# Performance work log

Hardware: AMD Instinct MI355X
Metric: run time of the kernel (lower is better)

## Reference

```python
import jax, jax.numpy as jnp
import numpy as np

COMMITMENT_COST = 0.25


def setup_inputs() -> dict:
    key = jax.random.key(0)
    kx, ke = jax.random.split(key)
    B, T, D = 64, 512, 256
    Q, K = 8, 1024
    x = jax.random.normal(kx, (B, T, D), dtype=jnp.float32)
    # matches nn.Embedding init uniform_(-1/codebook_size, 1/codebook_size)
    embeddings = jax.random.uniform(ke, (Q, K, D), dtype=jnp.float32,
                                    minval=-1.0 / K, maxval=1.0 / K)
    return {"x": x, "embeddings": embeddings}


def _vq_layer(residual, emb):
    # residual: [B,T,D], emb: [K,D]
    B, T, D = residual.shape
    flat = residual.reshape(-1, D)                               # [N,D]
    # squared distances via ||a||^2 + ||b||^2 - 2 a.b
    dist = (jnp.sum(flat * flat, axis=1, keepdims=True)
            + jnp.sum(emb * emb, axis=1)
            - 2.0 * (flat @ emb.T))                              # [N,K]
    idx = jnp.argmin(dist, axis=1)                               # [N]
    q = emb[idx].reshape(residual.shape)                         # gather == one_hot @ emb
    sg = jax.lax.stop_gradient
    e_latent = jnp.mean((sg(q) - residual) ** 2)
    q_latent = jnp.mean((q - sg(residual)) ** 2)
    loss = q_latent + COMMITMENT_COST * e_latent
    quantized = residual + sg(q - residual)                      # straight-through
    return quantized, loss, idx.reshape(B, T)


def reference(x, embeddings):
    # Residual VQ: sequentially quantize the residual with each codebook.
    def step(residual, emb):
        quantized, loss, idx = _vq_layer(residual, emb)
        return residual - quantized, (loss, idx)

    residual, (losses, indices) = jax.lax.scan(step, x, embeddings)
    output = x - residual                                        # [B,T,D]
    total_loss = jnp.sum(losses)
    return output, total_loss, indices                           # indices: [Q,B,T]
```

## Files before the change

### kernel.cpp

```cpp
#include <hip/hip_runtime.h>

#define NTOK   32768
#define DDIM   256
#define KCODES 1024
#define QLAYERS 8

#define MT     64
#define NCHUNK 32
#define NCH    (KCODES / NCHUNK)
#define DELTA  4e-4f
#define RPAD   260

typedef __attribute__((ext_vector_type(8))) _Float16 f16x8;
typedef __attribute__((ext_vector_type(4))) float f32x4;


__global__ void ce_kernel(const float* __restrict__ emb, float* __restrict__ ce) {
  int gid  = blockIdx.x * blockDim.x + threadIdx.x;
  int code = gid >> 6;
  int lane = threadIdx.x & 63;
  float4 v = reinterpret_cast<const float4*>(emb + (size_t)code * DDIM)[lane];
  float s = v.x * v.x + v.y * v.y + v.z * v.z + v.w * v.w;
#pragma unroll
  for (int off = 32; off; off >>= 1) s += __shfl_xor(s, off);
  if (lane == 0) ce[code] = s;
}

__global__ void split16_kernel(const float* __restrict__ emb, _Float16* __restrict__ eh) {
  int g  = blockIdx.x * blockDim.x + threadIdx.x;
  int c  = g >> 5;
  int dg = g & 31;
  const float4* p = reinterpret_cast<const float4*>(emb + (size_t)c * DDIM + dg * 8);
  float4 a = p[0], b = p[1];
  f16x8 h;
  h[0] = (_Float16)(a.x * 256.f); h[1] = (_Float16)(a.y * 256.f);
  h[2] = (_Float16)(a.z * 256.f); h[3] = (_Float16)(a.w * 256.f);
  h[4] = (_Float16)(b.x * 256.f); h[5] = (_Float16)(b.y * 256.f);
  h[6] = (_Float16)(b.z * 256.f); h[7] = (_Float16)(b.w * 256.f);
  *reinterpret_cast<f16x8*>(eh + (size_t)c * DDIM + (size_t)((dg ^ (c & 7)) * 8)) = h;
}

__device__ __forceinline__ void lexins(float d, int c, float v[3], int ci[3]) {
  bool l2 = (d < v[2]) || (d == v[2] && c < ci[2]);
  bool l1 = (d < v[1]) || (d == v[1] && c < ci[1]);
  bool l0 = (d < v[0]) || (d == v[0] && c < ci[0]);
  v[2] = l1 ? v[1] : (l2 ? d : v[2]);  ci[2] = l1 ? ci[1] : (l2 ? c : ci[2]);
  v[1] = l0 ? v[0] : (l1 ? d : v[1]);  ci[1] = l0 ? ci[0] : (l1 ? c : ci[1]);
  v[0] = l0 ? d : v[0];                ci[0] = l0 ? c : ci[0];
}

__device__ __forceinline__ void ins3(float d, int c, float v[3], int ci[3]) {
  bool l2 = d < v[2];
  bool l1 = d < v[1];
  bool l0 = d < v[0];
  v[2] = l1 ? v[1] : (l2 ? d : v[2]);  ci[2] = l1 ? ci[1] : (l2 ? c : ci[2]);
  v[1] = l0 ? v[0] : (l1 ? d : v[1]);  ci[1] = l0 ? ci[0] : (l1 ? c : ci[1]);
  v[0] = l0 ? d : v[0];                ci[0] = l0 ? c : ci[0];
}

__device__ __forceinline__ float exact_dist(const float* __restrict__ rrow,
                                            const float* __restrict__ erow,
                                            float cf, float cev) {
  float acc = 0.f;
  const float4* e4 = reinterpret_cast<const float4*>(erow);
  const float4* a4 = reinterpret_cast<const float4*>(rrow);
#pragma unroll 8
  for (int j = 0; j < 64; ++j) {
    float4 b = e4[j], a = a4[j];
    acc = fmaf(a.x, b.x, acc); acc = fmaf(a.y, b.y, acc);
    acc = fmaf(a.z, b.z, acc); acc = fmaf(a.w, b.w, acc);
  }
  float t1 = cf + cev;
  return t1 - 2.0f * acc;
}

__global__ __launch_bounds__(256, 1)
void vq_fused_kernel(const float* __restrict__ x, const float* __restrict__ emb,
                     const _Float16* __restrict__ eh16, const float* __restrict__ ce,
                     float* __restrict__ out, float* __restrict__ idx_out,
                     float* __restrict__ loss_part) {
  __shared__ __align__(16) float res_s[MT][RPAD];
  __shared__ __align__(16) _Float16 estage[2][NCHUNK * DDIM];
  __shared__ __align__(16) float ce_s[KCODES];
  __shared__ float cf_s[MT];
  __shared__ float t3v[MT][3];
  __shared__ int   t3i[MT][3];
  __shared__ int   idx_s[MT];
  __shared__ float rr_v[256];
  __shared__ int   rr_i[256];
  __shared__ unsigned long long fullmask;
  __shared__ float wsum[4];

  const int t    = threadIdx.x;
  const int lane = t & 63, w = t >> 6;
  const int l15  = lane & 15, lq = lane >> 4;
  const int tok0 = blockIdx.x * MT;

#pragma unroll
  for (int j = 0; j < 16; ++j) {
    int u = j * 256 + t;
    float4 xv = reinterpret_cast<const float4*>(x)[(size_t)blockIdx.x * 4096 + u];
    *reinterpret_cast<float4*>(&res_s[u >> 6][(u & 63) * 4]) = xv;
  }

  float lossacc = 0.f;

  for (int q = 0; q < QLAYERS; ++q) {
    const float*    embq = emb + (size_t)q * KCODES * DDIM;
    const _Float16* ehq  = eh16 + (size_t)q * KCODES * DDIM;
    const float*    ceq  = ce + (size_t)q * KCODES;

    __syncthreads();

    uint4 sreg[4];
#pragma unroll
    for (int i = 0; i < 4; ++i)
      sreg[i] = *reinterpret_cast<const uint4*>(ehq + i * 2048 + t * 8);

    reinterpret_cast<float4*>(ce_s)[t] = reinterpret_cast<const float4*>(ceq)[t];

    {
      const int m = t >> 2, p = t & 3;
      float s = 0.f;
#pragma unroll
      for (int j = 0; j < 16; ++j) {
        float4 v = *reinterpret_cast<const float4*>(&res_s[m][p * 64 + j * 4]);
        s = fmaf(v.x, v.x, s); s = fmaf(v.y, v.y, s);
        s = fmaf(v.z, v.z, s); s = fmaf(v.w, v.w, s);
      }
      s += __shfl_xor(s, 1);
      s += __shfl_xor(s, 2);
      if (p == 0) cf_s[m] = s;
    }

    f16x8 af[8];
#pragma unroll
    for (int ds = 0; ds < 8; ++ds) {
      const float* pr = &res_s[w * 16 + l15][ds * 32 + lq * 8];
      float4 a = *reinterpret_cast<const float4*>(pr);
      float4 b = *reinterpret_cast<const float4*>(pr + 4);
      f16x8 h;
      h[0] = (_Float16)a.x; h[1] = (_Float16)a.y; h[2] = (_Float16)a.z; h[3] = (_Float16)a.w;
      h[4] = (_Float16)b.x; h[5] = (_Float16)b.y; h[6] = (_Float16)b.z; h[7] = (_Float16)b.w;
      af[ds] = h;
    }

    __syncthreads();
#pragma unroll
    for (int i = 0; i < 4; ++i)
      *reinterpret_cast<uint4*>(&estage[0][i * 2048 + t * 8]) = sreg[i];
    __syncthreads();

    float cfreg[4];
#pragma unroll
    for (int r = 0; r < 4; ++r) cfreg[r] = cf_s[w * 16 + lq * 4 + r];

    float tv[4][3]; int ti[4][3];
#pragma unroll
    for (int s = 0; s < 4; ++s)
#pragma unroll
      for (int k = 0; k < 3; ++k) { tv[s][k] = 3.4e38f; ti[s][k] = 0; }

    for (int kc = 0; kc < NCH; ++kc) {
      const int buf = kc & 1;
      if (kc + 1 < NCH) {
        const _Float16* src = ehq + (size_t)(kc + 1) * NCHUNK * DDIM;
#pragma unroll
        for (int i = 0; i < 4; ++i)
          sreg[i] = *reinterpret_cast<const uint4*>(src + i * 2048 + t * 8);
      }

      f32x4 acc[2][2];
#pragma unroll
      for (int c2 = 0; c2 < 2; ++c2)
#pragma unroll
        for (int pp = 0; pp < 2; ++pp) acc[c2][pp] = (f32x4){0.f, 0.f, 0.f, 0.f};

      const _Float16* bb = estage[buf];
#pragma unroll
      for (int ds = 0; ds < 8; ++ds) {
        const int col = ds * 32 + lq * 8;
        const int r0  = l15;
        const int r1  = 16 + l15;
        f16x8 b0 = *reinterpret_cast<const f16x8*>(&bb[r0 * DDIM + (col ^ ((r0 & 7) * 8))]);
        f16x8 b1 = *reinterpret_cast<const f16x8*>(&bb[r1 * DDIM + (col ^ ((r1 & 7) * 8))]);
        acc[0][ds & 1] = __builtin_amdgcn_mfma_f32_16x16x32_f16(af[ds], b0, acc[0][ds & 1], 0, 0, 0);
        acc[1][ds & 1] = __builtin_amdgcn_mfma_f32_16x16x32_f16(af[ds], b1, acc[1][ds & 1], 0, 0, 0);
      }

#pragma unroll
      for (int c2 = 0; c2 < 2; ++c2) {
        const int   cg  = kc * NCHUNK + c2 * 16 + l15;
        const float cev = ce_s[cg];
#pragma unroll
        for (int r = 0; r < 4; ++r) {
          float dot = acc[c2][0][r] + acc[c2][1][r];
          float d   = fmaf(-0.0078125f, dot, cfreg[r] + cev);
          ins3(d, cg, tv[r], ti[r]);
        }
      }

      __syncthreads();
      if (kc + 1 < NCH) {
#pragma unroll
        for (int i = 0; i < 4; ++i)
          *reinterpret_cast<uint4*>(&estage[buf ^ 1][i * 2048 + t * 8]) = sreg[i];
      }
      __syncthreads();
    }

#pragma unroll
    for (int s = 0; s < 4; ++s) {
#pragma unroll
      for (int off = 1; off <= 8; off <<= 1) {
        float a0 = __shfl_xor(tv[s][0], off), a1 = __shfl_xor(tv[s][1], off),
              a2 = __shfl_xor(tv[s][2], off);
        int   b0 = __shfl_xor(ti[s][0], off), b1 = __shfl_xor(ti[s][1], off),
              b2 = __shfl_xor(ti[s][2], off);
        lexins(a0, b0, tv[s], ti[s]);
        lexins(a1, b1, tv[s], ti[s]);
        lexins(a2, b2, tv[s], ti[s]);
      }
      if (l15 == 0) {
        const int tok = w * 16 + lq * 4 + s;
        t3v[tok][0] = tv[s][0]; t3v[tok][1] = tv[s][1]; t3v[tok][2] = tv[s][2];
        t3i[tok][0] = ti[s][0]; t3i[tok][1] = ti[s][1]; t3i[tok][2] = ti[s][2];
      }
    }
    __syncthreads();

    if (t < MT) {
      float v0 = t3v[t][0], v1 = t3v[t][1], v2 = t3v[t][2];
      int   c0 = t3i[t][0], c1 = t3i[t][1];
      int best = c0;
      bool needfull = false;
      if (v1 - v0 >= DELTA) {
      } else if (v2 - v0 >= DELTA) {
        int ia = min(c0, c1), ib = max(c0, c1);
        float da = exact_dist(&res_s[t][0], embq + (size_t)ia * DDIM, cf_s[t], ce_s[ia]);
        float db = exact_dist(&res_s[t][0], embq + (size_t)ib * DDIM, cf_s[t], ce_s[ib]);
        best = (db < da) ? ib : ia;
      } else {
        needfull = true;
      }
      idx_s[t] = best;
      unsigned long long bm = __ballot(needfull);
      if (t == 0) fullmask = bm;
    }
    __syncthreads();

    unsigned long long fm = fullmask;
    while (fm) {
      const int f = __builtin_ctzll(fm);
      fm &= fm - 1;
      const float cfv = cf_s[f];
      float bestv = 3.4e38f; int besti = 0;
#pragma unroll
      for (int u = 0; u < 4; ++u) {
        int c = t * 4 + u;
        const float4* e4 = reinterpret_cast<const float4*>(embq + (size_t)c * DDIM);
        float acc = 0.f;
#pragma unroll 8
        for (int j = 0; j < 64; ++j) {
          float4 b = e4[j];
          float4 a = *reinterpret_cast<const float4*>(&res_s[f][j * 4]);
          acc = fmaf(a.x, b.x, acc); acc = fmaf(a.y, b.y, acc);
          acc = fmaf(a.z, b.z, acc); acc = fmaf(a.w, b.w, acc);
        }
        float dist = (cfv + ce_s[c]) - 2.0f * acc;
        if (dist < bestv) { bestv = dist; besti = c; }
      }
      rr_v[t] = bestv; rr_i[t] = besti;
      __syncthreads();
      if (t < 64) {
        float vb = rr_v[t]; int ib = rr_i[t];
#pragma unroll
        for (int s = 64; s < 256; s += 64) {
          float ov = rr_v[t + s]; int oi = rr_i[t + s];
          if (ov < vb || (ov == vb && oi < ib)) { vb = ov; ib = oi; }
        }
#pragma unroll
        for (int off = 1; off < 64; off <<= 1) {
          float ov = __shfl_xor(vb, off); int oi = __shfl_xor(ib, off);
          if (ov < vb || (ov == vb && oi < ib)) { vb = ov; ib = oi; }
        }
        if (t == 0) idx_s[f] = ib;
      }
      __syncthreads();
    }

    if (t < MT) idx_out[(size_t)q * NTOK + tok0 + t] = (float)idx_s[t];

    {
      const int m = t >> 2, p = t & 3;
      const int ci = idx_s[m];
      const float4* e4 = reinterpret_cast<const float4*>(embq + (size_t)ci * DDIM + p * 64);
      float s = 0.f;
#pragma unroll
      for (int j = 0; j < 16; ++j) {
        float4 e = e4[j];
        float4* rp = reinterpret_cast<float4*>(&res_s[m][p * 64 + j * 4]);
        float4 r = *rp;
        float4 nr = make_float4(r.x - e.x, r.y - e.y, r.z - e.z, r.w - e.w);
        s = fmaf(nr.x, nr.x, s); s = fmaf(nr.y, nr.y, s);
        s = fmaf(nr.z, nr.z, s); s = fmaf(nr.w, nr.w, s);
        *rp = nr;
      }
#pragma unroll
      for (int off = 32; off; off >>= 1) s += __shfl_xor(s, off);
      if ((t & 63) == 0) wsum[w] = s;
    }
    __syncthreads();
    if (t == 0) lossacc += wsum[0] + wsum[1] + wsum[2] + wsum[3];
  }

  __syncthreads();
#pragma unroll
  for (int j = 0; j < 16; ++j) {
    int u = j * 256 + t;
    float4 xv = reinterpret_cast<const float4*>(x)[(size_t)blockIdx.x * 4096 + u];
    float4 r = *reinterpret_cast<const float4*>(&res_s[u >> 6][(u & 63) * 4]);
    reinterpret_cast<float4*>(out)[(size_t)blockIdx.x * 4096 + u] =
        make_float4(xv.x - r.x, xv.y - r.y, xv.z - r.z, xv.w - r.w);
  }
  if (t == 0) loss_part[blockIdx.x] = lossacc;
}

__global__ void loss_final_kernel(const float* __restrict__ part, float* __restrict__ loss_out) {
  int t = threadIdx.x;
  float s = 0.f;
#pragma unroll
  for (int j = 0; j < 8; ++j) s += part[j * 64 + t];
#pragma unroll
  for (int off = 32; off; off >>= 1) s += __shfl_xor(s, off);
  if (t == 0) *loss_out = s * (1.25f / ((float)NTOK * (float)DDIM));
}

extern "C" void kernel_launch(void* const* d_in, const int* in_sizes, int n_in,
                              void* d_out, int out_size, void* d_ws, size_t ws_size,
                              hipStream_t stream) {
  const float* x   = (const float*)d_in[0];
  const float* emb = (const float*)d_in[1];
  float* out      = (float*)d_out;
  float* loss     = out + (size_t)NTOK * DDIM;
  float* idx_base = loss + 1;

  _Float16* eh16    = (_Float16*)d_ws;
  float* ce         = (float*)(eh16 + (size_t)QLAYERS * KCODES * DDIM);
  float* loss_part  = ce + (size_t)QLAYERS * KCODES;

  split16_kernel<<<QLAYERS * KCODES * 32 / 256, 256, 0, stream>>>(emb, eh16);
  ce_kernel<<<QLAYERS * KCODES * 64 / 256, 256, 0, stream>>>(emb, ce);
  vq_fused_kernel<<<NTOK / MT, 256, 0, stream>>>(x, emb, eh16, ce, out, idx_base, loss_part);
  loss_final_kernel<<<1, 64, 0, stream>>>(loss_part, loss);
}
```

Baseline: 1.278 ms.

## Load codebook fragments directly into registers, split waves over tokens and codes, track top-2

The codebook no longer passes through a double-buffered LDS stage. Each wave loads its B fragments straight from global memory into registers, with a one-chunk register prefetch, and the two per-chunk block barriers are removed. Waves are rearranged into a 2x2 split over token halves and code halves, so each B fragment feeds two MFMAs. The shared-memory drop allows a two-blocks-per-SM launch bound. The top-3 tracking and the two-candidate exact rescoring path are replaced by top-2, so any near tie now falls back to the full exact search, which may run more often; redundant global loads and register pressure also go up.

```diff
diff --git a/kernel.cpp b/kernel.cpp
--- a/kernel.cpp
+++ b/kernel.cpp
@@ -6,8 +6,8 @@
 #define QLAYERS 8
 
 #define MT     64
-#define NCHUNK 32
-#define NCH    (KCODES / NCHUNK)
+#define NCODE  32
+#define NCH    (KCODES / NCODE)
 #define DELTA  4e-4f
 #define RPAD   260
 
@@ -37,54 +37,33 @@
   h[2] = (_Float16)(a.z * 256.f); h[3] = (_Float16)(a.w * 256.f);
   h[4] = (_Float16)(b.x * 256.f); h[5] = (_Float16)(b.y * 256.f);
   h[6] = (_Float16)(b.z * 256.f); h[7] = (_Float16)(b.w * 256.f);
-  *reinterpret_cast<f16x8*>(eh + (size_t)c * DDIM + (size_t)((dg ^ (c & 7)) * 8)) = h;
-}
-
-__device__ __forceinline__ void lexins(float d, int c, float v[3], int ci[3]) {
-  bool l2 = (d < v[2]) || (d == v[2] && c < ci[2]);
+  *reinterpret_cast<f16x8*>(eh + (size_t)c * DDIM + (size_t)dg * 8) = h;
+}
+
+__device__ __forceinline__ void ins2(float d, int c, float v[2], int ci[2]) {
+  bool l1 = d < v[1];
+  bool l0 = d < v[0];
+  v[1] = l0 ? v[0] : (l1 ? d : v[1]);  ci[1] = l0 ? ci[0] : (l1 ? c : ci[1]);
+  v[0] = l0 ? d : v[0];                ci[0] = l0 ? c : ci[0];
+}
+
+__device__ __forceinline__ void lexins2(float d, int c, float v[2], int ci[2]) {
   bool l1 = (d < v[1]) || (d == v[1] && c < ci[1]);
   bool l0 = (d < v[0]) || (d == v[0] && c < ci[0]);
-  v[2] = l1 ? v[1] : (l2 ? d : v[2]);  ci[2] = l1 ? ci[1] : (l2 ? c : ci[2]);
   v[1] = l0 ? v[0] : (l1 ? d : v[1]);  ci[1] = l0 ? ci[0] : (l1 ? c : ci[1]);
   v[0] = l0 ? d : v[0];                ci[0] = l0 ? c : ci[0];
 }
 
-__device__ __forceinline__ void ins3(float d, int c, float v[3], int ci[3]) {
-  bool l2 = d < v[2];
-  bool l1 = d < v[1];
-  bool l0 = d < v[0];
-  v[2] = l1 ? v[1] : (l2 ? d : v[2]);  ci[2] = l1 ? ci[1] : (l2 ? c : ci[2]);
-  v[1] = l0 ? v[0] : (l1 ? d : v[1]);  ci[1] = l0 ? ci[0] : (l1 ? c : ci[1]);
-  v[0] = l0 ? d : v[0];                ci[0] = l0 ? c : ci[0];
-}
-
-__device__ __forceinline__ float exact_dist(const float* __restrict__ rrow,
-                                            const float* __restrict__ erow,
-                                            float cf, float cev) {
-  float acc = 0.f;
-  const float4* e4 = reinterpret_cast<const float4*>(erow);
-  const float4* a4 = reinterpret_cast<const float4*>(rrow);
-#pragma unroll 8
-  for (int j = 0; j < 64; ++j) {
-    float4 b = e4[j], a = a4[j];
-    acc = fmaf(a.x, b.x, acc); acc = fmaf(a.y, b.y, acc);
-    acc = fmaf(a.z, b.z, acc); acc = fmaf(a.w, b.w, acc);
-  }
-  float t1 = cf + cev;
-  return t1 - 2.0f * acc;
-}
-
-__global__ __launch_bounds__(256, 1)
+__global__ __launch_bounds__(256, 2)
 void vq_fused_kernel(const float* __restrict__ x, const float* __restrict__ emb,
                      const _Float16* __restrict__ eh16, const float* __restrict__ ce,
                      float* __restrict__ out, float* __restrict__ idx_out,
                      float* __restrict__ loss_part) {
   __shared__ __align__(16) float res_s[MT][RPAD];
-  __shared__ __align__(16) _Float16 estage[2][NCHUNK * DDIM];
   __shared__ __align__(16) float ce_s[KCODES];
   __shared__ float cf_s[MT];
-  __shared__ float t3v[MT][3];
-  __shared__ int   t3i[MT][3];
+  __shared__ float t2v[2][MT][2];
+  __shared__ int   t2i[2][MT][2];
   __shared__ int   idx_s[MT];
   __shared__ float rr_v[256];
   __shared__ int   rr_i[256];
@@ -93,6 +72,8 @@
 
   const int t    = threadIdx.x;
   const int lane = t & 63, w = t >> 6;
+  const int tg   = w & 1;
+  const int ch   = w >> 1;
   const int l15  = lane & 15, lq = lane >> 4;
   const int tok0 = blockIdx.x * MT;
 
@@ -112,11 +93,6 @@
 
     __syncthreads();
 
-    uint4 sreg[4];
-#pragma unroll
-    for (int i = 0; i < 4; ++i)
-      sreg[i] = *reinterpret_cast<const uint4*>(ehq + i * 2048 + t * 8);
-
     reinterpret_cast<float4*>(ce_s)[t] = reinterpret_cast<const float4*>(ceq)[t];
 
     {
@@ -133,118 +109,105 @@
       if (p == 0) cf_s[m] = s;
     }
 
-    f16x8 af[8];
-#pragma unroll
-    for (int ds = 0; ds < 8; ++ds) {
-      const float* pr = &res_s[w * 16 + l15][ds * 32 + lq * 8];
-      float4 a = *reinterpret_cast<const float4*>(pr);
-      float4 b = *reinterpret_cast<const float4*>(pr + 4);
-      f16x8 h;
-      h[0] = (_Float16)a.x; h[1] = (_Float16)a.y; h[2] = (_Float16)a.z; h[3] = (_Float16)a.w;
-      h[4] = (_Float16)b.x; h[5] = (_Float16)b.y; h[6] = (_Float16)b.z; h[7] = (_Float16)b.w;
-      af[ds] = h;
-    }
-
-    __syncthreads();
-#pragma unroll
-    for (int i = 0; i < 4; ++i)
-      *reinterpret_cast<uint4*>(&estage[0][i * 2048 + t * 8]) = sreg[i];
-    __syncthreads();
-
-    float cfreg[4];
-#pragma unroll
-    for (int r = 0; r < 4; ++r) cfreg[r] = cf_s[w * 16 + lq * 4 + r];
-
-    float tv[4][3]; int ti[4][3];
-#pragma unroll
-    for (int s = 0; s < 4; ++s)
-#pragma unroll
-      for (int k = 0; k < 3; ++k) { tv[s][k] = 3.4e38f; ti[s][k] = 0; }
+    f16x8 af[2][8];
+#pragma unroll
+    for (int mi = 0; mi < 2; ++mi)
+#pragma unroll
+      for (int ds = 0; ds < 8; ++ds) {
+        const float* pr = &res_s[tg * 32 + mi * 16 + l15][ds * 32 + lq * 8];
+        float4 a = *reinterpret_cast<const float4*>(pr);
+        float4 b = *reinterpret_cast<const float4*>(pr + 4);
+        f16x8 h;
+        h[0] = (_Float16)a.x; h[1] = (_Float16)a.y; h[2] = (_Float16)a.z; h[3] = (_Float16)a.w;
+        h[4] = (_Float16)b.x; h[5] = (_Float16)b.y; h[6] = (_Float16)b.z; h[7] = (_Float16)b.w;
+        af[mi][ds] = h;
+      }
+
+    __syncthreads();
+
+    float cfreg[2][4];
+#pragma unroll
+    for (int mi = 0; mi < 2; ++mi)
+#pragma unroll
+      for (int r = 0; r < 4; ++r) cfreg[mi][r] = cf_s[tg * 32 + mi * 16 + lq * 4 + r];
+
+    float tv[8][2]; int ti[8][2];
+#pragma unroll
+    for (int s = 0; s < 8; ++s) {
+      tv[s][0] = 3.4e38f; tv[s][1] = 3.4e38f; ti[s][0] = 0; ti[s][1] = 0;
+    }
+
+    const _Float16* bp = ehq + (size_t)(ch * 16 + l15) * DDIM + lq * 8;
+    uint4 bcur[8];
+#pragma unroll
+    for (int i = 0; i < 8; ++i)
+      bcur[i] = *reinterpret_cast<const uint4*>(bp + i * 32);
 
     for (int kc = 0; kc < NCH; ++kc) {
-      const int buf = kc & 1;
+      uint4 bnxt[8];
       if (kc + 1 < NCH) {
-        const _Float16* src = ehq + (size_t)(kc + 1) * NCHUNK * DDIM;
-#pragma unroll
-        for (int i = 0; i < 4; ++i)
-          sreg[i] = *reinterpret_cast<const uint4*>(src + i * 2048 + t * 8);
+        const _Float16* bnp = bp + (size_t)(kc + 1) * NCODE * DDIM;
+#pragma unroll
+        for (int i = 0; i < 8; ++i)
+          bnxt[i] = *reinterpret_cast<const uint4*>(bnp + i * 32);
       }
 
       f32x4 acc[2][2];
 #pragma unroll
-      for (int c2 = 0; c2 < 2; ++c2)
-#pragma unroll
-        for (int pp = 0; pp < 2; ++pp) acc[c2][pp] = (f32x4){0.f, 0.f, 0.f, 0.f};
-
-      const _Float16* bb = estage[buf];
+      for (int mi = 0; mi < 2; ++mi)
+#pragma unroll
+        for (int p = 0; p < 2; ++p) acc[mi][p] = (f32x4){0.f, 0.f, 0.f, 0.f};
+
 #pragma unroll
       for (int ds = 0; ds < 8; ++ds) {
-        const int col = ds * 32 + lq * 8;
-        const int r0  = l15;
-        const int r1  = 16 + l15;
-        f16x8 b0 = *reinterpret_cast<const f16x8*>(&bb[r0 * DDIM + (col ^ ((r0 & 7) * 8))]);
-        f16x8 b1 = *reinterpret_cast<const f16x8*>(&bb[r1 * DDIM + (col ^ ((r1 & 7) * 8))]);
-        acc[0][ds & 1] = __builtin_amdgcn_mfma_f32_16x16x32_f16(af[ds], b0, acc[0][ds & 1], 0, 0, 0);
-        acc[1][ds & 1] = __builtin_amdgcn_mfma_f32_16x16x32_f16(af[ds], b1, acc[1][ds & 1], 0, 0, 0);
-      }
-
-#pragma unroll
-      for (int c2 = 0; c2 < 2; ++c2) {
-        const int   cg  = kc * NCHUNK + c2 * 16 + l15;
-        const float cev = ce_s[cg];
+        f16x8 b = __builtin_bit_cast(f16x8, bcur[ds]);
+        acc[0][ds & 1] = __builtin_amdgcn_mfma_f32_16x16x32_f16(af[0][ds], b, acc[0][ds & 1], 0, 0, 0);
+        acc[1][ds & 1] = __builtin_amdgcn_mfma_f32_16x16x32_f16(af[1][ds], b, acc[1][ds & 1], 0, 0, 0);
+      }
+
+      const int   cg  = kc * NCODE + ch * 16 + l15;
+      const float cev = ce_s[cg];
+#pragma unroll
+      for (int mi = 0; mi < 2; ++mi)
 #pragma unroll
         for (int r = 0; r < 4; ++r) {
-          float dot = acc[c2][0][r] + acc[c2][1][r];
-          float d   = fmaf(-0.0078125f, dot, cfreg[r] + cev);
-          ins3(d, cg, tv[r], ti[r]);
+          float dot = acc[mi][0][r] + acc[mi][1][r];
+          float d   = fmaf(-0.0078125f, dot, cfreg[mi][r] + cev);
+          ins2(d, cg, tv[mi * 4 + r], ti[mi * 4 + r]);
         }
-      }
-
-      __syncthreads();
+
       if (kc + 1 < NCH) {
 #pragma unroll
-        for (int i = 0; i < 4; ++i)
-          *reinterpret_cast<uint4*>(&estage[buf ^ 1][i * 2048 + t * 8]) = sreg[i];
-      }
-      __syncthreads();
-    }
-
-#pragma unroll
-    for (int s = 0; s < 4; ++s) {
+        for (int i = 0; i < 8; ++i) bcur[i] = bnxt[i];
+      }
+    }
+
+#pragma unroll
+    for (int s = 0; s < 8; ++s) {
 #pragma unroll
       for (int off = 1; off <= 8; off <<= 1) {
-        float a0 = __shfl_xor(tv[s][0], off), a1 = __shfl_xor(tv[s][1], off),
-              a2 = __shfl_xor(tv[s][2], off);
-        int   b0 = __shfl_xor(ti[s][0], off), b1 = __shfl_xor(ti[s][1], off),
-              b2 = __shfl_xor(ti[s][2], off);
-        lexins(a0, b0, tv[s], ti[s]);
-        lexins(a1, b1, tv[s], ti[s]);
-        lexins(a2, b2, tv[s], ti[s]);
+        float a0 = __shfl_xor(tv[s][0], off), a1 = __shfl_xor(tv[s][1], off);
+        int   b0 = __shfl_xor(ti[s][0], off), b1 = __shfl_xor(ti[s][1], off);
+        lexins2(a0, b0, tv[s], ti[s]);
+        lexins2(a1, b1, tv[s], ti[s]);
       }
       if (l15 == 0) {
-        const int tok = w * 16 + lq * 4 + s;
-        t3v[tok][0] = tv[s][0]; t3v[tok][1] = tv[s][1]; t3v[tok][2] = tv[s][2];
-        t3i[tok][0] = ti[s][0]; t3i[tok][1] = ti[s][1]; t3i[tok][2] = ti[s][2];
+        const int mi = s >> 2, r = s & 3;
+        const int tok = tg * 32 + mi * 16 + lq * 4 + r;
+        t2v[ch][tok][0] = tv[s][0]; t2v[ch][tok][1] = tv[s][1];
+        t2i[ch][tok][0] = ti[s][0]; t2i[ch][tok][1] = ti[s][1];
       }
     }
     __syncthreads();
 
     if (t < MT) {
-      float v0 = t3v[t][0], v1 = t3v[t][1], v2 = t3v[t][2];
-      int   c0 = t3i[t][0], c1 = t3i[t][1];
-      int best = c0;
-      bool needfull = false;
-      if (v1 - v0 >= DELTA) {
-      } else if (v2 - v0 >= DELTA) {
-        int ia = min(c0, c1), ib = max(c0, c1);
-        float da = exact_dist(&res_s[t][0], embq + (size_t)ia * DDIM, cf_s[t], ce_s[ia]);
-        float db = exact_dist(&res_s[t][0], embq + (size_t)ib * DDIM, cf_s[t], ce_s[ib]);
-        best = (db < da) ? ib : ia;
-      } else {
-        needfull = true;
-      }
-      idx_s[t] = best;
-      unsigned long long bm = __ballot(needfull);
+      float v[2]; int ci[2];
+      v[0]  = t2v[0][t][0]; v[1]  = t2v[0][t][1];
+      ci[0] = t2i[0][t][0]; ci[1] = t2i[0][t][1];
+      lexins2(t2v[1][t][0], t2i[1][t][0], v, ci);
+      lexins2(t2v[1][t][1], t2i[1][t][1], v, ci);
+      idx_s[t] = ci[0];
+      unsigned long long bm = __ballot(v[1] - v[0] < DELTA);
       if (t == 0) fullmask = bm;
     }
     __syncthreads();
```

Result: slower. 3.515 ms (+175.0%).

## Split fused VQ kernel into per-layer launches with residual in global memory

Applied to the files above, without the earlier changes.

Replaces the single kernel that kept each block's 64-token residual in shared memory across all 8 codebook layers with one launch per layer, storing the residual in the output buffer in global memory. Dropping the large shared residual tile and raising launch bounds to 3 blocks per CU is meant to let more blocks run concurrently and hide latency, since the old grid of 512 single-resident blocks left CUs underused. In exchange it adds global round trips of the residual per layer, extra init/final copy kernels, and more launches; the exact-distance fallbacks now read rows from global memory.

```diff
diff --git a/kernel.cpp b/kernel.cpp
--- a/kernel.cpp
+++ b/kernel.cpp
@@ -9,7 +9,7 @@
 #define NCHUNK 32
 #define NCH    (KCODES / NCHUNK)
 #define DELTA  4e-4f
-#define RPAD   260
+#define NBLK   (NTOK / MT)
 
 typedef __attribute__((ext_vector_type(8))) _Float16 f16x8;
 typedef __attribute__((ext_vector_type(4))) float f32x4;
@@ -40,6 +40,11 @@
   *reinterpret_cast<f16x8*>(eh + (size_t)c * DDIM + (size_t)((dg ^ (c & 7)) * 8)) = h;
 }
 
+__global__ void init_kernel(const float* __restrict__ x, float* __restrict__ res) {
+  size_t i = (size_t)blockIdx.x * blockDim.x + threadIdx.x;
+  reinterpret_cast<float4*>(res)[i] = reinterpret_cast<const float4*>(x)[i];
+}
+
 __device__ __forceinline__ void lexins(float d, int c, float v[3], int ci[3]) {
   bool l2 = (d < v[2]) || (d == v[2] && c < ci[2]);
   bool l1 = (d < v[1]) || (d == v[1] && c < ci[1]);
@@ -74,12 +79,13 @@
   return t1 - 2.0f * acc;
 }
 
-__global__ __launch_bounds__(256, 1)
-void vq_fused_kernel(const float* __restrict__ x, const float* __restrict__ emb,
-                     const _Float16* __restrict__ eh16, const float* __restrict__ ce,
-                     float* __restrict__ out, float* __restrict__ idx_out,
+__global__ __launch_bounds__(256, 3)
+void vq_layer_kernel(const float* __restrict__ emb,
+                     const _Float16* __restrict__ eh16,
+                     const float* __restrict__ ce,
+                     float* __restrict__ res,
+                     float* __restrict__ idx_out,
                      float* __restrict__ loss_part) {
-  __shared__ __align__(16) float res_s[MT][RPAD];
   __shared__ __align__(16) _Float16 estage[2][NCHUNK * DDIM];
   __shared__ __align__(16) float ce_s[KCODES];
   __shared__ float cf_s[MT];
@@ -96,241 +102,224 @@
   const int l15  = lane & 15, lq = lane >> 4;
   const int tok0 = blockIdx.x * MT;
 
-#pragma unroll
-  for (int j = 0; j < 16; ++j) {
-    int u = j * 256 + t;
-    float4 xv = reinterpret_cast<const float4*>(x)[(size_t)blockIdx.x * 4096 + u];
-    *reinterpret_cast<float4*>(&res_s[u >> 6][(u & 63) * 4]) = xv;
-  }
-
-  float lossacc = 0.f;
-
-  for (int q = 0; q < QLAYERS; ++q) {
-    const float*    embq = emb + (size_t)q * KCODES * DDIM;
-    const _Float16* ehq  = eh16 + (size_t)q * KCODES * DDIM;
-    const float*    ceq  = ce + (size_t)q * KCODES;
+  uint4 sreg[4];
+#pragma unroll
+  for (int i = 0; i < 4; ++i)
+    sreg[i] = *reinterpret_cast<const uint4*>(eh16 + i * 2048 + t * 8);
+
+  reinterpret_cast<float4*>(ce_s)[t] = reinterpret_cast<const float4*>(ce)[t];
+
+  {
+    const int m = t >> 2, p = t & 3;
+    const float4* r4 =
+        reinterpret_cast<const float4*>(res + (size_t)(tok0 + m) * DDIM + p * 64);
+    float s = 0.f;
+#pragma unroll
+    for (int j = 0; j < 16; ++j) {
+      float4 v = r4[j];
+      s = fmaf(v.x, v.x, s); s = fmaf(v.y, v.y, s);
+      s = fmaf(v.z, v.z, s); s = fmaf(v.w, v.w, s);
+    }
+    s += __shfl_xor(s, 1);
+    s += __shfl_xor(s, 2);
+    if (p == 0) cf_s[m] = s;
+  }
+
+  f16x8 af[8];
+#pragma unroll
+  for (int ds = 0; ds < 8; ++ds) {
+    const float* pr = res + (size_t)(tok0 + w * 16 + l15) * DDIM + ds * 32 + lq * 8;
+    float4 a = *reinterpret_cast<const float4*>(pr);
+    float4 b = *reinterpret_cast<const float4*>(pr + 4);
+    f16x8 h;
+    h[0] = (_Float16)a.x; h[1] = (_Float16)a.y; h[2] = (_Float16)a.z; h[3] = (_Float16)a.w;
+    h[4] = (_Float16)b.x; h[5] = (_Float16)b.y; h[6] = (_Float16)b.z; h[7] = (_Float16)b.w;
+    af[ds] = h;
+  }
+
+  __syncthreads();
+#pragma unroll
+  for (int i = 0; i < 4; ++i)
+    *reinterpret_cast<uint4*>(&estage[0][i * 2048 + t * 8]) = sreg[i];
+  __syncthreads();
+
+  float cfreg[4];
+#pragma unroll
+  for (int r = 0; r < 4; ++r) cfreg[r] = cf_s[w * 16 + lq * 4 + r];
+
+  float tv[4][3]; int ti[4][3];
+#pragma unroll
+  for (int s = 0; s < 4; ++s)
+#pragma unroll
+    for (int k = 0; k < 3; ++k) { tv[s][k] = 3.4e38f; ti[s][k] = 0; }
+
+  for (int kc = 0; kc < NCH; ++kc) {
+    const int buf = kc & 1;
+    if (kc + 1 < NCH) {
+      const _Float16* src = eh16 + (size_t)(kc + 1) * NCHUNK * DDIM;
+#pragma unroll
+      for (int i = 0; i < 4; ++i)
+        sreg[i] = *reinterpret_cast<const uint4*>(src + i * 2048 + t * 8);
+    }
+
+    f32x4 acc[2][2];
+#pragma unroll
+    for (int c2 = 0; c2 < 2; ++c2)
+#pragma unroll
+      for (int pp = 0; pp < 2; ++pp) acc[c2][pp] = (f32x4){0.f, 0.f, 0.f, 0.f};
+
+    const _Float16* bb = estage[buf];
+#pragma unroll
+    for (int ds = 0; ds < 8; ++ds) {
+      const int col = ds * 32 + lq * 8;
+      const int r0  = l15;
+      const int r1  = 16 + l15;
+      f16x8 b0 = *reinterpret_cast<const f16x8*>(&bb[r0 * DDIM + (col ^ ((r0 & 7) * 8))]);
+      f16x8 b1 = *reinterpret_cast<const f16x8*>(&bb[r1 * DDIM + (col ^ ((r1 & 7) * 8))]);
+      acc[0][ds & 1] = __builtin_amdgcn_mfma_f32_16x16x32_f16(af[ds], b0, acc[0][ds & 1], 0, 0, 0);
+      acc[1][ds & 1] = __builtin_amdgcn_mfma_f32_16x16x32_f16(af[ds], b1, acc[1][ds & 1], 0, 0, 0);
+    }
+
+#pragma unroll
+    for (int c2 = 0; c2 < 2; ++c2) {
+      const int   cg  = kc * NCHUNK + c2 * 16 + l15;
+      const float cev = ce_s[cg];
+#pragma unroll
+      for (int r = 0; r < 4; ++r) {
+        float dot = acc[c2][0][r] + acc[c2][1][r];
+        float d   = fmaf(-0.0078125f, dot, cfreg[r] + cev);
+        ins3(d, cg, tv[r], ti[r]);
+      }
+    }
 
     __syncthreads();
-
-    uint4 sreg[4];
-#pragma unroll
-    for (int i = 0; i < 4; ++i)
-      sreg[i] = *reinterpret_cast<const uint4*>(ehq + i * 2048 + t * 8);
-
-    reinterpret_cast<float4*>(ce_s)[t] = reinterpret_cast<const float4*>(ceq)[t];
-
-    {
-      const int m = t >> 2, p = t & 3;
-      float s = 0.f;
-#pragma unroll
-      for (int j = 0; j < 16; ++j) {
-        float4 v = *reinterpret_cast<const float4*>(&res_s[m][p * 64 + j * 4]);
-        s = fmaf(v.x, v.x, s); s = fmaf(v.y, v.y, s);
-        s = fmaf(v.z, v.z, s); s = fmaf(v.w, v.w, s);
+    if (kc + 1 < NCH) {
+#pragma unroll
+      for (int i = 0; i < 4; ++i)
+        *reinterpret_cast<uint4*>(&estage[buf ^ 1][i * 2048 + t * 8]) = sreg[i];
+    }
+    __syncthreads();
+  }
+
+#pragma unroll
+  for (int s = 0; s < 4; ++s) {
+#pragma unroll
+    for (int off = 1; off <= 8; off <<= 1) {
+      float a0 = __shfl_xor(tv[s][0], off), a1 = __shfl_xor(tv[s][1], off),
+            a2 = __shfl_xor(tv[s][2], off);
+      int   b0 = __shfl_xor(ti[s][0], off), b1 = __shfl_xor(ti[s][1], off),
+            b2 = __shfl_xor(ti[s][2], off);
+      lexins(a0, b0, tv[s], ti[s]);
+      lexins(a1, b1, tv[s], ti[s]);
+      lexins(a2, b2, tv[s], ti[s]);
+    }
+    if (l15 == 0) {
+      const int tok = w * 16 + lq * 4 + s;
+      t3v[tok][0] = tv[s][0]; t3v[tok][1] = tv[s][1]; t3v[tok][2] = tv[s][2];
+      t3i[tok][0] = ti[s][0]; t3i[tok][1] = ti[s][1]; t3i[tok][2] = ti[s][2];
+    }
+  }
+  __syncthreads();
+
+  if (t < MT) {
+    float v0 = t3v[t][0], v1 = t3v[t][1], v2 = t3v[t][2];
+    int   c0 = t3i[t][0], c1 = t3i[t][1];
+    int best = c0;
+    bool needfull = false;
+    if (v1 - v0 >= DELTA) {
+    } else if (v2 - v0 >= DELTA) {
+      const float* rrow = res + (size_t)(tok0 + t) * DDIM;
+      int ia = min(c0, c1), ib = max(c0, c1);
+      float da = exact_dist(rrow, emb + (size_t)ia * DDIM, cf_s[t], ce_s[ia]);
+      float db = exact_dist(rrow, emb + (size_t)ib * DDIM, cf_s[t], ce_s[ib]);
+      best = (db < da) ? ib : ia;
+    } else {
+      needfull = true;
+    }
+    idx_s[t] = best;
+    unsigned long long bm = __ballot(needfull);
+    if (t == 0) fullmask = bm;
+  }
+  __syncthreads();
+
+  unsigned long long fm = fullmask;
+  while (fm) {
+    const int f = __builtin_ctzll(fm);
+    fm &= fm - 1;
+    const float cfv = cf_s[f];
+    const float* rrow = res + (size_t)(tok0 + f) * DDIM;
+    float bestv = 3.4e38f; int besti = 0;
+#pragma unroll
+    for (int u = 0; u < 4; ++u) {
+      int c = t * 4 + u;
+      const float4* e4 = reinterpret_cast<const float4*>(emb + (size_t)c * DDIM);
+      float acc = 0.f;
+#pragma unroll 8
+      for (int j = 0; j < 64; ++j) {
+        float4 b = e4[j];
+        float4 a = *reinterpret_cast<const float4*>(rrow + j * 4);
+        acc = fmaf(a.x, b.x, acc); acc = fmaf(a.y, b.y, acc);
+        acc = fmaf(a.z, b.z, acc); acc = fmaf(a.w, b.w, acc);
       }
-      s += __shfl_xor(s, 1);
-      s += __shfl_xor(s, 2);
-      if (p == 0) cf_s[m] = s;
-    }
-
-    f16x8 af[8];
-#pragma unroll
-    for (int ds = 0; ds < 8; ++ds) {
-      const float* pr = &res_s[w * 16 + l15][ds * 32 + lq * 8];
-      float4 a = *reinterpret_cast<const float4*>(pr);
-      float4 b = *reinterpret_cast<const float4*>(pr + 4);
-      f16x8 h;
-      h[0] = (_Float16)a.x; h[1] = (_Float16)a.y; h[2] = (_Float16)a.z; h[3] = (_Float16)a.w;
-      h[4] = (_Float16)b.x; h[5] = (_Float16)b.y; h[6] = (_Float16)b.z; h[7] = (_Float16)b.w;
-      af[ds] = h;
-    }
-
+      float dist = (cfv + ce_s[c]) - 2.0f * acc;
+      if (dist < bestv) { bestv = dist; besti = c; }
+    }
+    rr_v[t] = bestv; rr_i[t] = besti;
     __syncthreads();
-#pragma unroll
-    for (int i = 0; i < 4; ++i)
-      *reinterpret_cast<uint4*>(&estage[0][i * 2048 + t * 8]) = sreg[i];
+    if (t < 64) {
+      float vb = rr_v[t]; int ib = rr_i[t];
+#pragma unroll
+      for (int s = 64; s < 256; s += 64) {
+        float ov = rr_v[t + s]; int oi = rr_i[t + s];
+        if (ov < vb || (ov == vb && oi < ib)) { vb = ov; ib = oi; }
+      }
+#pragma unroll
+      for (int off = 1; off < 64; off <<= 1) {
+        float ov = __shfl_xor(vb, off); int oi = __shfl_xor(ib, off);
+        if (ov < vb || (ov == vb && oi < ib)) { vb = ov; ib = oi; }
+      }
+      if (t == 0) idx_s[f] = ib;
+    }
     __syncthreads();
-
-    float cfreg[4];
-#pragma unroll
-    for (int r = 0; r < 4; ++r) cfreg[r] = cf_s[w * 16 + lq * 4 + r];
-
-    float tv[4][3]; int ti[4][3];
-#pragma unroll
-    for (int s = 0; s < 4; ++s)
-#pragma unroll
-      for (int k = 0; k < 3; ++k) { tv[s][k] = 3.4e38f; ti[s][k] = 0; }
-
-    for (int kc = 0; kc < NCH; ++kc) {
-      const int buf = kc & 1;
-      if (kc + 1 < NCH) {
-        const _Float16* src = ehq + (size_t)(kc + 1) * NCHUNK * DDIM;
-#pragma unroll
-        for (int i = 0; i < 4; ++i)
-          sreg[i] = *reinterpret_cast<const uint4*>(src + i * 2048 + t * 8);
-      }
-
-      f32x4 acc[2][2];
-#pragma unroll
-      for (int c2 = 0; c2 < 2; ++c2)
-#pragma unroll
-        for (int pp = 0; pp < 2; ++pp) acc[c2][pp] = (f32x4){0.f, 0.f, 0.f, 0.f};
-
-      const _Float16* bb = estage[buf];
-#pragma unroll
-      for (int ds = 0; ds < 8; ++ds) {
-        const int col = ds * 32 + lq * 8;
-        const int r0  = l15;
-        const int r1  = 16 + l15;
-        f16x8 b0 = *reinterpret_cast<const f16x8*>(&bb[r0 * DDIM + (col ^ ((r0 & 7) * 8))]);
-        f16x8 b1 = *reinterpret_cast<const f16x8*>(&bb[r1 * DDIM + (col ^ ((r1 & 7) * 8))]);
-        acc[0][ds & 1] = __builtin_amdgcn_mfma_f32_16x16x32_f16(af[ds], b0, acc[0][ds & 1], 0, 0, 0);
-        acc[1][ds & 1] = __builtin_amdgcn_mfma_f32_16x16x32_f16(af[ds], b1, acc[1][ds & 1], 0, 0, 0);
-      }
-
-#pragma unroll
-      for (int c2 = 0; c2 < 2; ++c2) {
-        const int   cg  = kc * NCHUNK + c2 * 16 + l15;
-        const float cev = ce_s[cg];
-#pragma unroll
-        for (int r = 0; r < 4; ++r) {
-          float dot = acc[c2][0][r] + acc[c2][1][r];
-          float d   = fmaf(-0.0078125f, dot, cfreg[r] + cev);
-          ins3(d, cg, tv[r], ti[r]);
-        }
-      }
-
-      __syncthreads();
-      if (kc + 1 < NCH) {
-#pragma unroll
-        for (int i = 0; i < 4; ++i)
-          *reinterpret_cast<uint4*>(&estage[buf ^ 1][i * 2048 + t * 8]) = sreg[i];
-      }
-      __syncthreads();
-    }
-
-#pragma unroll
-    for (int s = 0; s < 4; ++s) {
-#pragma unroll
-      for (int off = 1; off <= 8; off <<= 1) {
-        float a0 = __shfl_xor(tv[s][0], off), a1 = __shfl_xor(tv[s][1], off),
-              a2 = __shfl_xor(tv[s][2], off);
-        int   b0 = __shfl_xor(ti[s][0], off), b1 = __shfl_xor(ti[s][1], off),
-              b2 = __shfl_xor(ti[s][2], off);
-        lexins(a0, b0, tv[s], ti[s]);
-        lexins(a1, b1, tv[s], ti[s]);
-        lexins(a2, b2, tv[s], ti[s]);
-      }
-      if (l15 == 0) {
-        const int tok = w * 16 + lq * 4 + s;
-        t3v[tok][0] = tv[s][0]; t3v[tok][1] = tv[s][1]; t3v[tok][2] = tv[s][2];
-        t3i[tok][0] = ti[s][0]; t3i[tok][1] = ti[s][1]; t3i[tok][2] = ti[s][2];
-      }
-    }
-    __syncthreads();
-
-    if (t < MT) {
-      float v0 = t3v[t][0], v1 = t3v[t][1], v2 = t3v[t][2];
-      int   c0 = t3i[t][0], c1 = t3i[t][1];
-      int best = c0;
-      bool needfull = false;
-      if (v1 - v0 >= DELTA) {
-      } else if (v2 - v0 >= DELTA) {
-        int ia = min(c0, c1), ib = max(c0, c1);
-        float da = exact_dist(&res_s[t][0], embq + (size_t)ia * DDIM, cf_s[t], ce_s[ia]);
-        float db = exact_dist(&res_s[t][0], embq + (size_t)ib * DDIM, cf_s[t], ce_s[ib]);
-        best = (db < da) ? ib : ia;
-      } else {
-        needfull = true;
-      }
-      idx_s[t] = best;
-      unsigned long long bm = __ballot(needfull);
-      if (t == 0) fullmask = bm;
-    }
-    __syncthreads();
-
-    unsigned long long fm = fullmask;
-    while (fm) {
-      const int f = __builtin_ctzll(fm);
-      fm &= fm - 1;
-      const float cfv = cf_s[f];
-      float bestv = 3.4e38f; int besti = 0;
-#pragma unroll
-      for (int u = 0; u < 4; ++u) {
-        int c = t * 4 + u;
-        const float4* e4 = reinterpret_cast<const float4*>(embq + (size_t)c * DDIM);
-        float acc = 0.f;
-#pragma unroll 8
-        for (int j = 0; j < 64; ++j) {
-          float4 b = e4[j];
-          float4 a = *reinterpret_cast<const float4*>(&res_s[f][j * 4]);
-          acc = fmaf(a.x, b.x, acc); acc = fmaf(a.y, b.y, acc);
-          acc = fmaf(a.z, b.z, acc); acc = fmaf(a.w, b.w, acc);
-        }
-        float dist = (cfv + ce_s[c]) - 2.0f * acc;
-        if (dist < bestv) { bestv = dist; besti = c; }
-      }
-      rr_v[t] = bestv; rr_i[t] = besti;
-      __syncthreads();
-      if (t < 64) {
-        float vb = rr_v[t]; int ib = rr_i[t];
-#pragma unroll
-        for (int s = 64; s < 256; s += 64) {
-          float ov = rr_v[t + s]; int oi = rr_i[t + s];
-          if (ov < vb || (ov == vb && oi < ib)) { vb = ov; ib = oi; }
-        }
-#pragma unroll
-        for (int off = 1; off < 64; off <<= 1) {
-          float ov = __shfl_xor(vb, off); int oi = __shfl_xor(ib, off);
-          if (ov < vb || (ov == vb && oi < ib)) { vb = ov; ib = oi; }
-        }
-        if (t == 0) idx_s[f] = ib;
-      }
-      __syncthreads();
-    }
-
-    if (t < MT) idx_out[(size_t)q * NTOK + tok0 + t] = (float)idx_s[t];
-
-    {
-      const int m = t >> 2, p = t & 3;
-      const int ci = idx_s[m];
-      const float4* e4 = reinterpret_cast<const float4*>(embq + (size_t)ci * DDIM + p * 64);
-      float s = 0.f;
-#pragma unroll
-      for (int j = 0; j < 16; ++j) {
-        float4 e = e4[j];
-        float4* rp = reinterpret_cast<float4*>(&res_s[m][p * 64 + j * 4]);
-        float4 r = *rp;
-        float4 nr = make_float4(r.x - e.x, r.y - e.y, r.z - e.z, r.w - e.w);
-        s = fmaf(nr.x, nr.x, s); s = fmaf(nr.y, nr.y, s);
-        s = fmaf(nr.z, nr.z, s); s = fmaf(nr.w, nr.w, s);
-        *rp = nr;
-      }
-#pragma unroll
-      for (int off = 32; off; off >>= 1) s += __shfl_xor(s, off);
-      if ((t & 63) == 0) wsum[w] = s;
-    }
-    __syncthreads();
-    if (t == 0) lossacc += wsum[0] + wsum[1] + wsum[2] + wsum[3];
-  }
-
-  __syncthreads();
-#pragma unroll
-  for (int j = 0; j < 16; ++j) {
-    int u = j * 256 + t;
-    float4 xv = reinterpret_cast<const float4*>(x)[(size_t)blockIdx.x * 4096 + u];
-    float4 r = *reinterpret_cast<const float4*>(&res_s[u >> 6][(u & 63) * 4]);
-    reinterpret_cast<float4*>(out)[(size_t)blockIdx.x * 4096 + u] =
-        make_float4(xv.x - r.x, xv.y - r.y, xv.z - r.z, xv.w - r.w);
-  }
-  if (t == 0) loss_part[blockIdx.x] = lossacc;
+  }
+
+  if (t < MT) idx_out[tok0 + t] = (float)idx_s[t];
+
+  {
+    const int m = t >> 2, p = t & 3;
+    const int ci = idx_s[m];
+    const float4* e4 = reinterpret_cast<const float4*>(emb + (size_t)ci * DDIM + p * 64);
+    float4* r4 = reinterpret_cast<float4*>(res + (size_t)(tok0 + m) * DDIM + p * 64);
+    float s = 0.f;
+#pragma unroll
+    for (int j = 0; j < 16; ++j) {
+      float4 r = r4[j], e = e4[j];
+      float4 nr = make_float4(r.x - e.x, r.y - e.y, r.z - e.z, r.w - e.w);
+      s = fmaf(nr.x, nr.x, s); s = fmaf(nr.y, nr.y, s);
+      s = fmaf(nr.z, nr.z, s); s = fmaf(nr.w, nr.w, s);
+      r4[j] = nr;
+    }
+#pragma unroll
+    for (int off = 32; off; off >>= 1) s += __shfl_xor(s, off);
+    if ((t & 63) == 0) wsum[w] = s;
+  }
+  __syncthreads();
+  if (t == 0) loss_part[blockIdx.x] = wsum[0] + wsum[1] + wsum[2] + wsum[3];
+}
+
+__global__ void final_kernel(const float* __restrict__ x, float* __restrict__ out) {
+  size_t i = (size_t)blockIdx.x * blockDim.x + threadIdx.x;
+  float4 xv = reinterpret_cast<const float4*>(x)[i];
+  float4 r  = reinterpret_cast<float4*>(out)[i];
+  reinterpret_cast<float4*>(out)[i] =
+      make_float4(xv.x - r.x, xv.y - r.y, xv.z - r.z, xv.w - r.w);
 }
 
 __global__ void loss_final_kernel(const float* __restrict__ part, float* __restrict__ loss_out) {
   int t = threadIdx.x;
   float s = 0.f;
 #pragma unroll
-  for (int j = 0; j < 8; ++j) s += part[j * 64 + t];
+  for (int j = 0; j < QLAYERS * NBLK / 64; ++j) s += part[j * 64 + t];
 #pragma unroll
   for (int off = 32; off; off >>= 1) s += __shfl_xor(s, off);
   if (t == 0) *loss_out = s * (1.25f / ((float)NTOK * (float)DDIM));
@@ -345,12 +334,19 @@
   float* loss     = out + (size_t)NTOK * DDIM;
   float* idx_base = loss + 1;
 
-  _Float16* eh16    = (_Float16*)d_ws;
-  float* ce         = (float*)(eh16 + (size_t)QLAYERS * KCODES * DDIM);
-  float* loss_part  = ce + (size_t)QLAYERS * KCODES;
+  _Float16* eh16   = (_Float16*)d_ws;
+  float* ce        = (float*)(eh16 + (size_t)QLAYERS * KCODES * DDIM);
+  float* loss_part = ce + (size_t)QLAYERS * KCODES;
 
   split16_kernel<<<QLAYERS * KCODES * 32 / 256, 256, 0, stream>>>(emb, eh16);
   ce_kernel<<<QLAYERS * KCODES * 64 / 256, 256, 0, stream>>>(emb, ce);
-  vq_fused_kernel<<<NTOK / MT, 256, 0, stream>>>(x, emb, eh16, ce, out, idx_base, loss_part);
+  init_kernel<<<NTOK * DDIM / 4 / 256, 256, 0, stream>>>(x, out);
+  for (int q = 0; q < QLAYERS; ++q) {
+    vq_layer_kernel<<<NBLK, 256, 0, stream>>>(
+        emb + (size_t)q * KCODES * DDIM, eh16 + (size_t)q * KCODES * DDIM,
+        ce + (size_t)q * KCODES, out,
+        idx_base + (size_t)q * NTOK, loss_part + (size_t)q * NBLK);
+  }
+  final_kernel<<<NTOK * DDIM / 4 / 256, 256, 0, stream>>>(x, out);
   loss_final_kernel<<<1, 64, 0, stream>>>(loss_part, loss);
 }
```

Result: slower. 2.015 ms (+57.7%).
